# Optimization experiments

Hardware: AMD Instinct MI355X
Metric: run time of the kernel (lower is better)

## Reference

```python
import jax, jax.numpy as jnp
import numpy as np

N, E, D, L, G, C = 20000, 320000, 512, 6, 64, 10
EPS = 1e-5


def setup_inputs() -> dict:
    key = jax.random.key(0)
    ks = jax.random.split(key, 8)
    s = 0.05  # small init scale to keep activations sane across 6 layers
    x = jax.random.normal(ks[0], (N, D), jnp.float32)
    edge_index = jax.random.randint(ks[1], (2, E), 0, N, jnp.int32)
    batch = jnp.sort(jax.random.randint(ks[2], (N,), 0, G, jnp.int32))
    W_rel = jax.random.normal(ks[3], (L, D, D), jnp.float32) * s
    b_rel = jnp.zeros((L, D), jnp.float32)
    W_root = jax.random.normal(ks[4], (L, D, D), jnp.float32) * s
    gamma = jnp.ones((L, D), jnp.float32)
    beta = jnp.zeros((L, D), jnp.float32)
    lin_w = jax.random.normal(ks[5], (D, C), jnp.float32) * s
    lin_b = jnp.zeros((C,), jnp.float32)
    return {"x": x, "edge_index": edge_index, "batch": batch,
            "W_rel": W_rel, "b_rel": b_rel, "W_root": W_root,
            "gamma": gamma, "beta": beta, "lin_w": lin_w, "lin_b": lin_b}


def reference(x, edge_index, batch, W_rel, b_rel, W_root, gamma, beta, lin_w, lin_b):
    # PyG GraphConv (aggr='add'): out = segment_sum(x[src] -> dst) @ W_rel + b_rel + x @ W_root
    src, dst = edge_index[0], edge_index[1]
    n = x.shape[0]
    for l in range(W_rel.shape[0]):  # 6 structurally identical layers
        agg = jax.ops.segment_sum(x[src], dst, num_segments=n)  # [N, D]
        h = agg @ W_rel[l] + b_rel[l] + x @ W_root[l]
        # BatchNorm1d in training mode: biased batch statistics over nodes
        mu = jnp.mean(h, axis=0)
        var = jnp.mean(jnp.square(h - mu), axis=0)
        x = jax.nn.relu((h - mu) * jax.lax.rsqrt(var + EPS) * gamma[l] + beta[l])
    # global_mean_pool over per-node graph ids
    sums = jax.ops.segment_sum(x, batch, num_segments=G)              # [G, D]
    counts = jax.ops.segment_sum(jnp.ones((n,), x.dtype), batch, num_segments=G)
    pooled = sums / jnp.maximum(counts, 1.0)[:, None]
    return pooled @ lin_w + lin_b  # [G, C]
```

## Files before the change

### kernel.cpp

```cpp
#include <hip/hip_runtime.h>


typedef unsigned short u16;
typedef unsigned int u32;
typedef __attribute__((ext_vector_type(8))) short bf16x8;
typedef __attribute__((ext_vector_type(16))) float f32x16;
typedef __attribute__((ext_vector_type(2))) float f32x2;

#define DFEAT 512
#define KDIM 1024
#define NLAYER 6
#define NGRAPH 64
#define NCLS 10
#define BN_EPS 1e-5f
#define NBUCKET 1024

__device__ __forceinline__ float bf_lo(u32 u) { union { u32 i; float f; } v; v.i = u << 16; return v.f; }
__device__ __forceinline__ float bf_hi(u32 u) { union { u32 i; float f; } v; v.i = u & 0xFFFF0000u; return v.f; }
__device__ __forceinline__ u16 f2bf(float f) {
  union { float f; u32 i; } v; v.f = f;
  u32 r = v.i + 0x7FFFu + ((v.i >> 16) & 1u);
  return (u16)(r >> 16);
}
__device__ __forceinline__ u32 pack2(float lo, float hi) {
  return (u32)f2bf(lo) | ((u32)f2bf(hi) << 16);
}

__device__ __forceinline__ void gload_lds16(const u16* g, u16* lds_base) {
  __builtin_amdgcn_global_load_lds(
      (const __attribute__((address_space(1))) u32*)g,
      (__attribute__((address_space(3))) u32*)lds_base, 16, 0, 0);
}

__global__ void prep_kernel(const int* __restrict__ ei, int* __restrict__ counts, int E,
                            const float* __restrict__ Wrel, const float* __restrict__ Wroot,
                            u16* __restrict__ Wt,
                            const float* __restrict__ x, u16* __restrict__ A, int M,
                            int histB, int wB) {
  __shared__ float tile[64][65];
  int b = blockIdx.x;
  int tid = threadIdx.x;
  if (b < histB) {
    int e = b * 256 + tid;
    if (e < E) atomicAdd(&counts[ei[E + e]], 1);
  } else if (b < histB + wB) {
    int t = b - histB;
    int l = t >> 7;
    int tt = t & 127;
    int k0 = (tt >> 3) << 6;
    int n0 = (tt & 7) << 6;
    int rr = tid >> 4;
    int c4 = (tid & 15) << 2;
#pragma unroll
    for (int i = 0; i < 4; i++) {
      int k = k0 + i * 16 + rr;
      const float* src = (k < DFEAT)
          ? &Wrel[((size_t)l * DFEAT + k) * DFEAT + n0 + c4]
          : &Wroot[((size_t)l * DFEAT + (k - DFEAT)) * DFEAT + n0 + c4];
      float4 v = *(const float4*)src;
      float* d = &tile[i * 16 + rr][c4];
      d[0] = v.x; d[1] = v.y; d[2] = v.z; d[3] = v.w;
    }
    __syncthreads();
    int nr = tid >> 3;
    int kc = (tid & 7) << 3;
#pragma unroll
    for (int i = 0; i < 2; i++) {
      int nl = i * 32 + nr;
      uint4 o;
      o.x = pack2(tile[kc + 0][nl], tile[kc + 1][nl]);
      o.y = pack2(tile[kc + 2][nl], tile[kc + 3][nl]);
      o.z = pack2(tile[kc + 4][nl], tile[kc + 5][nl]);
      o.w = pack2(tile[kc + 6][nl], tile[kc + 7][nl]);
      *(uint4*)&Wt[(size_t)(l * DFEAT + n0 + nl) * KDIM + k0 + kc] = o;
    }
  } else {
    int idx = (b - histB - wB) * 256 + tid;
    int row = idx >> 7;
    int c4 = (idx & 127) * 4;
    if (row < M) {
      float4 v = *(const float4*)&x[(size_t)row * DFEAT + c4];
      uint2 o; o.x = pack2(v.x, v.y); o.y = pack2(v.z, v.w);
      *(uint2*)&A[(size_t)row * KDIM + DFEAT + c4] = o;
    }
  }
}

__global__ __launch_bounds__(1024) void dscan_kernel(const int* __restrict__ counts,
                                                     int* __restrict__ base0,
                                                     int* __restrict__ bcur,
                                                     int* __restrict__ edgebase,
                                                     int* __restrict__ row_ptr2, int n) {
  __shared__ int hist[NBUCKET];
  __shared__ int part[NBUCKET];
  int tid = threadIdx.x;
  hist[tid] = 0;
  __syncthreads();
  for (int i = tid; i < n; i += 1024) {
    int d = counts[i]; if (d > NBUCKET - 1) d = NBUCKET - 1;
    atomicAdd(&hist[d], 1);
  }
  __syncthreads();
  int c = hist[tid];
  part[tid] = c; __syncthreads();
  int x = c;
  for (int off = 1; off < NBUCKET; off <<= 1) {
    int t = (tid >= off) ? part[tid - off] : 0;
    __syncthreads();
    x += t; part[tid] = x;
    __syncthreads();
  }
  base0[tid] = x - c;
  bcur[tid] = x - c;
  int w = c * tid;
  part[tid] = w; __syncthreads();
  int y = w;
  for (int off = 1; off < NBUCKET; off <<= 1) {
    int t = (tid >= off) ? part[tid - off] : 0;
    __syncthreads();
    y += t; part[tid] = y;
    __syncthreads();
  }
  edgebase[tid] = y - w;
  if (tid == NBUCKET - 1) row_ptr2[n] = y;
}

__global__ __launch_bounds__(256) void rank_kernel(const int* __restrict__ counts,
                                                   const int* __restrict__ base0,
                                                   int* __restrict__ bcur,
                                                   const int* __restrict__ edgebase,
                                                   int* __restrict__ perm,
                                                   int* __restrict__ row_ptr2,
                                                   int* __restrict__ cursor2, int n) {
  __shared__ int hb[NBUCKET];
  __shared__ int hstart[NBUCKET];
  int tid = threadIdx.x;
  for (int d = tid; d < NBUCKET; d += 256) hb[d] = 0;
  __syncthreads();
  int row = blockIdx.x * 256 + tid;
  bool valid = (row < n);
  int deg = 0, j = 0;
  if (valid) {
    deg = counts[row]; if (deg > NBUCKET - 1) deg = NBUCKET - 1;
    j = atomicAdd(&hb[deg], 1);
  }
  __syncthreads();
  for (int d = tid; d < NBUCKET; d += 256) {
    int c = hb[d];
    hstart[d] = c ? atomicAdd(&bcur[d], c) : 0;
  }
  __syncthreads();
  if (valid) {
    int rnk = hstart[deg] + j;
    int jj = rnk - base0[deg];
    int v = edgebase[deg] + jj * deg;
    perm[rnk] = row;
    row_ptr2[rnk] = v;
    cursor2[row] = v;
  }
}

__global__ void scatter_kernel(const int* __restrict__ ei, int* __restrict__ cursor2,
                               int* __restrict__ csr2, int E) {
  int e = blockIdx.x * 256 + threadIdx.x;
  if (e < E) {
    int d = ei[E + e];
    int pos = atomicAdd(&cursor2[d], 1);
    csr2[pos] = ei[e];
  }
}

template <bool FUSED>
__device__ __forceinline__ void acc8(uint4 v, const f32x2* sc, const f32x2* sh, f32x2* a) {
  f32x2 t0 = {bf_lo(v.x), bf_hi(v.x)};
  f32x2 t1 = {bf_lo(v.y), bf_hi(v.y)};
  f32x2 t2 = {bf_lo(v.z), bf_hi(v.z)};
  f32x2 t3 = {bf_lo(v.w), bf_hi(v.w)};
  if constexpr (FUSED) {
    f32x2 z = {0.f, 0.f};
    a[0] += __builtin_elementwise_max(t0 * sc[0] + sh[0], z);
    a[1] += __builtin_elementwise_max(t1 * sc[1] + sh[1], z);
    a[2] += __builtin_elementwise_max(t2 * sc[2] + sh[2], z);
    a[3] += __builtin_elementwise_max(t3 * sc[3] + sh[3], z);
  } else {
    a[0] += t0; a[1] += t1; a[2] += t2; a[3] += t3;
  }
}

#define GCAP 1536
template <bool FUSED>
__global__ __launch_bounds__(256) void gather_kernel(u16* __restrict__ A,
                                                     const u16* __restrict__ Hb,
                                                     const float* __restrict__ sums,
                                                     const float* __restrict__ gamma,
                                                     const float* __restrict__ beta,
                                                     const int* __restrict__ row_ptr2,
                                                     const int* __restrict__ csr2,
                                                     const int* __restrict__ perm,
                                                     int n, float invN) {
  __shared__ int sidx[GCAP];
  int b = blockIdx.x;
  int slice = b & 7;
  int grp = b >> 3;
  int tid = threadIdx.x;
  int r0 = grp * 32;
  int rend = (r0 + 32 < n) ? (r0 + 32) : n;
  int wbeg = row_ptr2[r0], wend = row_ptr2[rend];
  int cnt = wend - wbeg;
  bool lds_ok = (cnt <= GCAP);
  if (lds_ok)
    for (int t = tid; t < cnt; t += 256) sidx[t] = csr2[wbeg + t];
  __syncthreads();

  int wid = tid >> 6, lane = tid & 63;
  int dsub = lane >> 3, fl = lane & 7;
  int rnk = r0 + wid * 8 + dsub;
  if (rnk >= n) return;
  int dst = perm[rnk];
  int cc = slice * 64 + fl * 8;
  f32x2 sc2[4], sh2[4];
  if constexpr (FUSED) {
#pragma unroll
    for (int j = 0; j < 8; j++) {
      int c = cc + j;
      float mu = sums[c] * invN;
      float var = sums[DFEAT + c] * invN - mu * mu;
      float s = gamma[c] * rsqrtf(var + BN_EPS);
      sc2[j >> 1][j & 1] = s;
      sh2[j >> 1][j & 1] = beta[c] - mu * s;
    }
    uint4 h = *(const uint4*)&Hb[(size_t)dst * DFEAT + cc];
    f32x2 z = {0.f, 0.f};
    f32x2 e0 = __builtin_elementwise_max((f32x2){bf_lo(h.x), bf_hi(h.x)} * sc2[0] + sh2[0], z);
    f32x2 e1 = __builtin_elementwise_max((f32x2){bf_lo(h.y), bf_hi(h.y)} * sc2[1] + sh2[1], z);
    f32x2 e2 = __builtin_elementwise_max((f32x2){bf_lo(h.z), bf_hi(h.z)} * sc2[2] + sh2[2], z);
    f32x2 e3 = __builtin_elementwise_max((f32x2){bf_lo(h.w), bf_hi(h.w)} * sc2[3] + sh2[3], z);
    uint4 o;
    o.x = pack2(e0[0], e0[1]); o.y = pack2(e1[0], e1[1]);
    o.z = pack2(e2[0], e2[1]); o.w = pack2(e3[0], e3[1]);
    *(uint4*)&A[(size_t)dst * KDIM + DFEAT + cc] = o;
  }
  const u16* Sx = FUSED ? (Hb + cc) : (A + DFEAT + cc);
  const size_t RS = FUSED ? DFEAT : KDIM;
  int db = row_ptr2[rnk], de = row_ptr2[rnk + 1];
  f32x2 a[4] = {};
  if (lds_ok) {
    int e = db - wbeg, ee = de - wbeg;
    for (; e + 7 < ee; e += 8) {
      int s0 = sidx[e + 0], s1 = sidx[e + 1], s2 = sidx[e + 2], s3 = sidx[e + 3];
      int s4 = sidx[e + 4], s5 = sidx[e + 5], s6 = sidx[e + 6], s7 = sidx[e + 7];
      uint4 v0 = *(const uint4*)&Sx[(size_t)s0 * RS];
      uint4 v1 = *(const uint4*)&Sx[(size_t)s1 * RS];
      uint4 v2 = *(const uint4*)&Sx[(size_t)s2 * RS];
      uint4 v3 = *(const uint4*)&Sx[(size_t)s3 * RS];
      uint4 v4 = *(const uint4*)&Sx[(size_t)s4 * RS];
      uint4 v5 = *(const uint4*)&Sx[(size_t)s5 * RS];
      uint4 v6 = *(const uint4*)&Sx[(size_t)s6 * RS];
      uint4 v7 = *(const uint4*)&Sx[(size_t)s7 * RS];
      acc8<FUSED>(v0, sc2, sh2, a); acc8<FUSED>(v1, sc2, sh2, a);
      acc8<FUSED>(v2, sc2, sh2, a); acc8<FUSED>(v3, sc2, sh2, a);
      acc8<FUSED>(v4, sc2, sh2, a); acc8<FUSED>(v5, sc2, sh2, a);
      acc8<FUSED>(v6, sc2, sh2, a); acc8<FUSED>(v7, sc2, sh2, a);
    }
    for (; e < ee; ++e) {
      uint4 v = *(const uint4*)&Sx[(size_t)sidx[e] * RS];
      acc8<FUSED>(v, sc2, sh2, a);
    }
  } else {
    for (int e = db; e < de; ++e) {
      uint4 v = *(const uint4*)&Sx[(size_t)csr2[e] * RS];
      acc8<FUSED>(v, sc2, sh2, a);
    }
  }
  uint4 o;
  o.x = pack2(a[0][0], a[0][1]); o.y = pack2(a[1][0], a[1][1]);
  o.z = pack2(a[2][0], a[2][1]); o.w = pack2(a[3][0], a[3][1]);
  *(uint4*)&A[(size_t)dst * KDIM + cc] = o;
}

#define BM 128
#define BN 128
#define BK 64
#define CSTR 132
__global__ __launch_bounds__(256, 4) void gemm_kernel(const u16* __restrict__ A,
                                                      const u16* __restrict__ Bt,
                                                      const float* __restrict__ bias,
                                                      u16* __restrict__ Hb,
                                                      float* __restrict__ sums, int M) {
  const int lin = blockIdx.x;
  const int bx = ((lin >> 5) << 3) + (lin & 7);
  const int by = (lin >> 3) & 3;
  const int m0 = bx * BM;
  if (m0 >= M) return;
  const int n0 = by * BN;

  __shared__ u16 smem[BM * CSTR];
  __shared__ float sred[2 * BN];
  u16* As = smem;
  u16* Bs = smem + BM * BK;
  const int tid = threadIdx.x;
  const int wid = tid >> 6, lane = tid & 63;
  const int wm = wid >> 1, wn = wid & 1;
  const int l31 = lane & 31, half = lane >> 5;

  if (tid < 2 * BN) sred[tid] = 0.f;

  const int dr = lane >> 3;
  const int gcol = ((lane & 7) ^ dr) * 8;
  int arow[4], brow[4];
#pragma unroll
  for (int t = 0; t < 4; t++) {
    int r = wid * 32 + t * 8 + dr;
    int ar = m0 + r; if (ar >= M) ar = M - 1;
    arow[t] = ar;
    brow[t] = n0 + r;
  }

  f32x16 acc[2][2] = {};

  for (int k0 = 0; k0 < KDIM; k0 += BK) {
    __syncthreads();
#pragma unroll
    for (int t = 0; t < 4; t++)
      gload_lds16(&A[(size_t)arow[t] * KDIM + k0 + gcol], &As[(wid * 32 + t * 8) * BK]);
#pragma unroll
    for (int t = 0; t < 4; t++)
      gload_lds16(&Bt[(size_t)brow[t] * KDIM + k0 + gcol], &Bs[(wid * 32 + t * 8) * BK]);
    __syncthreads();
#pragma unroll
    for (int ks = 0; ks < 4; ks++) {
      int slot = ((ks * 2 + half) ^ (l31 & 7)) * 8;
      bf16x8 a0 = *(const bf16x8*)&As[(wm * 64 + l31) * BK + slot];
      bf16x8 a1 = *(const bf16x8*)&As[(wm * 64 + 32 + l31) * BK + slot];
      bf16x8 b0 = *(const bf16x8*)&Bs[(wn * 64 + l31) * BK + slot];
      bf16x8 b1 = *(const bf16x8*)&Bs[(wn * 64 + 32 + l31) * BK + slot];
      acc[0][0] = __builtin_amdgcn_mfma_f32_32x32x16_bf16(a0, b0, acc[0][0], 0, 0, 0);
      acc[0][1] = __builtin_amdgcn_mfma_f32_32x32x16_bf16(a0, b1, acc[0][1], 0, 0, 0);
      acc[1][0] = __builtin_amdgcn_mfma_f32_32x32x16_bf16(a1, b0, acc[1][0], 0, 0, 0);
      acc[1][1] = __builtin_amdgcn_mfma_f32_32x32x16_bf16(a1, b1, acc[1][1], 0, 0, 0);
    }
  }

  __syncthreads();

#pragma unroll
  for (int nt = 0; nt < 2; nt++) {
    int colt = wn * 64 + nt * 32 + l31;
    float bv = bias[n0 + colt];
    float s = 0.f, s2 = 0.f;
#pragma unroll
    for (int mt = 0; mt < 2; mt++) {
      int rbase = wm * 64 + mt * 32 + half * 4;
#pragma unroll
      for (int reg = 0; reg < 16; reg++) {
        int rowt = rbase + (reg & 3) + 8 * (reg >> 2);
        float v = acc[mt][nt][reg] + bv;
        smem[rowt * CSTR + colt] = f2bf(v);
        if (m0 + rowt < M) { s += v; s2 += v * v; }
      }
    }
    s  += __shfl_xor(s, 32);
    s2 += __shfl_xor(s2, 32);
    if (half == 0) {
      atomicAdd(&sred[colt], s);
      atomicAdd(&sred[BN + colt], s2);
    }
  }
  __syncthreads();

  const int rsub = tid >> 4;
  const int c8 = (tid & 15) * 8;
#pragma unroll
  for (int it = 0; it < 8; it++) {
    int rowt = it * 16 + rsub;
    int grow = m0 + rowt;
    if (grow < M) {
      uint4 v = *(const uint4*)&smem[rowt * CSTR + c8];
      *(uint4*)&Hb[(size_t)grow * DFEAT + n0 + c8] = v;
    }
  }
  if (tid < BN) {
    atomicAdd(&sums[n0 + tid], sred[tid]);
    atomicAdd(&sums[DFEAT + n0 + tid], sred[BN + tid]);
  }
}

__device__ __forceinline__ int lower_bound_dev(const int* a, int n, int v) {
  int lo = 0, hi = n;
  while (lo < hi) { int mid = (lo + hi) >> 1; if (a[mid] < v) lo = mid + 1; else hi = mid; }
  return lo;
}

__global__ __launch_bounds__(1024) void pool_kernel(const u16* __restrict__ Hb,
                                                    const float* __restrict__ sums,
                                                    const float* __restrict__ gamma,
                                                    const float* __restrict__ beta,
                                                    const int* __restrict__ batch,
                                                    float* __restrict__ pooled, int n, float invN) {
  __shared__ float red[DFEAT];
  int g = blockIdx.x;
  int tid = threadIdx.x;
  if (tid < DFEAT) red[tid] = 0.f;
  int lo = lower_bound_dev(batch, n, g);
  int hi = lower_bound_dev(batch, n, g + 1);
  int rowOff = tid >> 6, lane = tid & 63;
  int c0 = lane * 8;
  float sc[8], sh[8];
#pragma unroll
  for (int j = 0; j < 8; j++) {
    int c = c0 + j;
    float mu = sums[c] * invN;
    float var = sums[DFEAT + c] * invN - mu * mu;
    float s = gamma[c] * rsqrtf(var + BN_EPS);
    sc[j] = s;
    sh[j] = beta[c] - mu * s;
  }
  float a[8] = {};
  for (int r = lo + rowOff; r < hi; r += 16) {
    uint4 v = *(const uint4*)&Hb[(size_t)r * DFEAT + c0];
    float e0 = bf_lo(v.x), e1 = bf_hi(v.x), e2 = bf_lo(v.y), e3 = bf_hi(v.y);
    float e4 = bf_lo(v.z), e5 = bf_hi(v.z), e6 = bf_lo(v.w), e7 = bf_hi(v.w);
    a[0] += fmaxf(e0 * sc[0] + sh[0], 0.f); a[1] += fmaxf(e1 * sc[1] + sh[1], 0.f);
    a[2] += fmaxf(e2 * sc[2] + sh[2], 0.f); a[3] += fmaxf(e3 * sc[3] + sh[3], 0.f);
    a[4] += fmaxf(e4 * sc[4] + sh[4], 0.f); a[5] += fmaxf(e5 * sc[5] + sh[5], 0.f);
    a[6] += fmaxf(e6 * sc[6] + sh[6], 0.f); a[7] += fmaxf(e7 * sc[7] + sh[7], 0.f);
  }
  __syncthreads();
#pragma unroll
  for (int j = 0; j < 8; j++) atomicAdd(&red[c0 + j], a[j]);
  __syncthreads();
  if (tid < DFEAT) pooled[g * DFEAT + tid] = red[tid] / fmaxf((float)(hi - lo), 1.0f);
}

__global__ __launch_bounds__(64) void final_kernel(const float* __restrict__ pooled,
                                                   const float* __restrict__ lin_w,
                                                   const float* __restrict__ lin_b,
                                                   float* __restrict__ out) {
  int g = blockIdx.x;
  int lane = threadIdx.x;
  float acc[NCLS] = {};
  float4 p0 = *(const float4*)&pooled[g * DFEAT + lane * 8];
  float4 p1 = *(const float4*)&pooled[g * DFEAT + lane * 8 + 4];
  float pv[8] = {p0.x, p0.y, p0.z, p0.w, p1.x, p1.y, p1.z, p1.w};
#pragma unroll
  for (int j = 0; j < 8; j++) {
    int k = lane * 8 + j;
#pragma unroll
    for (int c = 0; c < NCLS; c++) acc[c] += pv[j] * lin_w[k * NCLS + c];
  }
#pragma unroll
  for (int off = 32; off > 0; off >>= 1)
#pragma unroll
    for (int c = 0; c < NCLS; c++) acc[c] += __shfl_down(acc[c], off);
  if (lane == 0)
#pragma unroll
    for (int c = 0; c < NCLS; c++) out[g * NCLS + c] = acc[c] + lin_b[c];
}

extern "C" void kernel_launch(void* const* d_in, const int* in_sizes, int n_in,
                              void* d_out, int out_size, void* d_ws, size_t ws_size,
                              hipStream_t stream) {
  const float* x      = (const float*)d_in[0];
  const int*   ei     = (const int*)d_in[1];
  const int*   batch  = (const int*)d_in[2];
  const float* W_rel  = (const float*)d_in[3];
  const float* b_rel  = (const float*)d_in[4];
  const float* W_root = (const float*)d_in[5];
  const float* gamma  = (const float*)d_in[6];
  const float* beta   = (const float*)d_in[7];
  const float* lin_w  = (const float*)d_in[8];
  const float* lin_b  = (const float*)d_in[9];
  float* out = (float*)d_out;

  const int N = in_sizes[0] / DFEAT;
  const int E = in_sizes[1] / 2;

  char* p = (char*)d_ws;
  u16*   A        = (u16*)p;    p += (size_t)N * KDIM * 2;
  u16*   Hb       = (u16*)p;    p += (size_t)N * DFEAT * 2;
  u16*   Wt       = (u16*)p;    p += (size_t)NLAYER * DFEAT * KDIM * 2;
  int*   row_ptr2 = (int*)p;    p += ((size_t)(N + 1) * 4 + 15) / 16 * 16;
  int*   counts   = (int*)p;    p += (size_t)N * 4;
  int*   cursor2  = (int*)p;    p += (size_t)N * 4;
  int*   perm     = (int*)p;    p += (size_t)N * 4;
  int*   csr2     = (int*)p;    p += (size_t)E * 4;
  int*   base0    = (int*)p;    p += (size_t)NBUCKET * 4;
  int*   bcur     = (int*)p;    p += (size_t)NBUCKET * 4;
  int*   edgebase = (int*)p;    p += (size_t)NBUCKET * 4;
  float* sums     = (float*)p;  p += (size_t)NLAYER * 2 * DFEAT * 4;
  float* pooled   = (float*)p;  p += (size_t)NGRAPH * DFEAT * 4;

  const float invN = 1.0f / (float)N;

  hipMemsetAsync(counts, 0, (size_t)N * 4, stream);
  hipMemsetAsync(sums, 0, (size_t)NLAYER * 2 * DFEAT * 4, stream);

  const int histB = (E + 255) / 256;
  const int wB = NLAYER * 128;
  const int xB = (N * 128 + 255) / 256;
  prep_kernel<<<histB + wB + xB, 256, 0, stream>>>(ei, counts, E, W_rel, W_root, Wt,
                                                   x, A, N, histB, wB);
  dscan_kernel<<<1, 1024, 0, stream>>>(counts, base0, bcur, edgebase, row_ptr2, N);
  rank_kernel<<<(N + 255) / 256, 256, 0, stream>>>(counts, base0, bcur, edgebase,
                                                   perm, row_ptr2, cursor2, N);
  scatter_kernel<<<(E + 255) / 256, 256, 0, stream>>>(ei, cursor2, csr2, E);

  const int ngrp8 = ((N + 31) / 32) * 8;
  const int gtiles = (((N + BM - 1) / BM + 7) / 8) * 8 * 4;

  for (int l = 0; l < NLAYER; ++l) {
    float* sums_l = sums + (size_t)l * 2 * DFEAT;
    if (l == 0)
      gather_kernel<false><<<ngrp8, 256, 0, stream>>>(A, Hb, nullptr, nullptr, nullptr,
                                                      row_ptr2, csr2, perm, N, invN);
    else
      gather_kernel<true><<<ngrp8, 256, 0, stream>>>(A, Hb,
          sums + (size_t)(l - 1) * 2 * DFEAT,
          gamma + (size_t)(l - 1) * DFEAT, beta + (size_t)(l - 1) * DFEAT,
          row_ptr2, csr2, perm, N, invN);
    gemm_kernel<<<gtiles, 256, 0, stream>>>(A, Wt + (size_t)l * DFEAT * KDIM,
                                            b_rel + (size_t)l * DFEAT, Hb, sums_l, N);
  }

  pool_kernel<<<NGRAPH, 1024, 0, stream>>>(Hb, sums + (size_t)(NLAYER - 1) * 2 * DFEAT,
                                           gamma + (size_t)(NLAYER - 1) * DFEAT,
                                           beta + (size_t)(NLAYER - 1) * DFEAT,
                                           batch, pooled, N, invN);
  final_kernel<<<NGRAPH, 64, 0, stream>>>(pooled, lin_w, lin_b, out);
}
```

Baseline: 562.3 us.

## Double-buffer GEMM LDS tiles and reverse gather block order

Measured after the change: 621.7 us. 1.11x slower.

```diff
diff --git a/kernel.cpp b/kernel.cpp
--- a/kernel.cpp
+++ b/kernel.cpp
@@ -201,7 +201,8 @@
   __shared__ int sidx[GCAP];
   int b = blockIdx.x;
   int slice = b & 7;
-  int grp = b >> 3;
+  int nGrp = (n + 31) >> 5;
+  int grp = nGrp - 1 - (b >> 3);
   int tid = threadIdx.x;
   int r0 = grp * 32;
   int rend = (r0 + 32 < n) ? (r0 + 32) : n;
@@ -282,7 +283,8 @@
 #define BN 128
 #define BK 64
 #define CSTR 132
-__global__ __launch_bounds__(256, 4) void gemm_kernel(const u16* __restrict__ A,
+#define BUFSZ (BM * BK + BN * BK)
+__global__ __launch_bounds__(256, 2) void gemm_kernel(const u16* __restrict__ A,
                                                       const u16* __restrict__ Bt,
                                                       const float* __restrict__ bias,
                                                       u16* __restrict__ Hb,
@@ -294,10 +296,8 @@
   if (m0 >= M) return;
   const int n0 = by * BN;
 
-  __shared__ u16 smem[BM * CSTR];
+  __shared__ u16 smem[2 * BUFSZ];
   __shared__ float sred[2 * BN];
-  u16* As = smem;
-  u16* Bs = smem + BM * BK;
   const int tid = threadIdx.x;
   const int wid = tid >> 6, lane = tid & 63;
   const int wm = wid >> 1, wn = wid & 1;
@@ -318,30 +318,42 @@
 
   f32x16 acc[2][2] = {};
 
-  for (int k0 = 0; k0 < KDIM; k0 += BK) {
-    __syncthreads();
-#pragma unroll
-    for (int t = 0; t < 4; t++)
-      gload_lds16(&A[(size_t)arow[t] * KDIM + k0 + gcol], &As[(wid * 32 + t * 8) * BK]);
-#pragma unroll
-    for (int t = 0; t < 4; t++)
-      gload_lds16(&Bt[(size_t)brow[t] * KDIM + k0 + gcol], &Bs[(wid * 32 + t * 8) * BK]);
-    __syncthreads();
+#pragma unroll
+  for (int t = 0; t < 4; t++) {
+    gload_lds16(&A[(size_t)arow[t] * KDIM + gcol], &smem[(wid * 32 + t * 8) * BK]);
+    gload_lds16(&Bt[(size_t)brow[t] * KDIM + gcol], &smem[BM * BK + (wid * 32 + t * 8) * BK]);
+  }
+  __syncthreads();
+
+  const int NIT = KDIM / BK;
+  for (int it = 0; it < NIT; ++it) {
+    const int cur = it & 1;
+    if (it + 1 < NIT) {
+      const int k1 = (it + 1) * BK;
+      u16* Asn = &smem[(cur ^ 1) * BUFSZ];
+      u16* Bsn = Asn + BM * BK;
+#pragma unroll
+      for (int t = 0; t < 4; t++) {
+        gload_lds16(&A[(size_t)arow[t] * KDIM + k1 + gcol], &Asn[(wid * 32 + t * 8) * BK]);
+        gload_lds16(&Bt[(size_t)brow[t] * KDIM + k1 + gcol], &Bsn[(wid * 32 + t * 8) * BK]);
+      }
+    }
+    const u16* Asc = &smem[cur * BUFSZ];
+    const u16* Bsc = Asc + BM * BK;
 #pragma unroll
     for (int ks = 0; ks < 4; ks++) {
       int slot = ((ks * 2 + half) ^ (l31 & 7)) * 8;
-      bf16x8 a0 = *(const bf16x8*)&As[(wm * 64 + l31) * BK + slot];
-      bf16x8 a1 = *(const bf16x8*)&As[(wm * 64 + 32 + l31) * BK + slot];
-      bf16x8 b0 = *(const bf16x8*)&Bs[(wn * 64 + l31) * BK + slot];
-      bf16x8 b1 = *(const bf16x8*)&Bs[(wn * 64 + 32 + l31) * BK + slot];
+      bf16x8 a0 = *(const bf16x8*)&Asc[(wm * 64 + l31) * BK + slot];
+      bf16x8 a1 = *(const bf16x8*)&Asc[(wm * 64 + 32 + l31) * BK + slot];
+      bf16x8 b0 = *(const bf16x8*)&Bsc[(wn * 64 + l31) * BK + slot];
+      bf16x8 b1 = *(const bf16x8*)&Bsc[(wn * 64 + 32 + l31) * BK + slot];
       acc[0][0] = __builtin_amdgcn_mfma_f32_32x32x16_bf16(a0, b0, acc[0][0], 0, 0, 0);
       acc[0][1] = __builtin_amdgcn_mfma_f32_32x32x16_bf16(a0, b1, acc[0][1], 0, 0, 0);
       acc[1][0] = __builtin_amdgcn_mfma_f32_32x32x16_bf16(a1, b0, acc[1][0], 0, 0, 0);
       acc[1][1] = __builtin_amdgcn_mfma_f32_32x32x16_bf16(a1, b1, acc[1][1], 0, 0, 0);
     }
-  }
-
-  __syncthreads();
+    __syncthreads();
+  }
 
 #pragma unroll
   for (int nt = 0; nt < 2; nt++) {
```

## Widen GEMM tile to 128x256 with 512 threads and reverse gather block order

Applied to the files above, without the earlier changes.

New measurement: 586.2 us. +4.2%, slower.

```diff
diff --git a/kernel.cpp b/kernel.cpp
--- a/kernel.cpp
+++ b/kernel.cpp
@@ -201,7 +201,8 @@
   __shared__ int sidx[GCAP];
   int b = blockIdx.x;
   int slice = b & 7;
-  int grp = b >> 3;
+  int nGrp = (n + 31) >> 5;
+  int grp = nGrp - 1 - (b >> 3);
   int tid = threadIdx.x;
   int r0 = grp * 32;
   int rend = (r0 + 32 < n) ? (r0 + 32) : n;
@@ -279,50 +280,51 @@
 }
 
 #define BM 128
-#define BN 128
+#define BN 256
 #define BK 64
 #define CSTR 132
-__global__ __launch_bounds__(256, 4) void gemm_kernel(const u16* __restrict__ A,
+__global__ __launch_bounds__(512, 4) void gemm_kernel(const u16* __restrict__ A,
                                                       const u16* __restrict__ Bt,
                                                       const float* __restrict__ bias,
                                                       u16* __restrict__ Hb,
                                                       float* __restrict__ sums, int M) {
   const int lin = blockIdx.x;
-  const int bx = ((lin >> 5) << 3) + (lin & 7);
-  const int by = (lin >> 3) & 3;
+  const int bx = ((lin >> 4) << 3) + (lin & 7);
+  const int by = (lin >> 3) & 1;
   const int m0 = bx * BM;
   if (m0 >= M) return;
   const int n0 = by * BN;
 
-  __shared__ u16 smem[BM * CSTR];
+  __shared__ u16 smem[BM * BK + BN * BK];
   __shared__ float sred[2 * BN];
   u16* As = smem;
   u16* Bs = smem + BM * BK;
   const int tid = threadIdx.x;
   const int wid = tid >> 6, lane = tid & 63;
-  const int wm = wid >> 1, wn = wid & 1;
+  const int wm = wid >> 2, wn = wid & 3;
   const int l31 = lane & 31, half = lane >> 5;
 
   if (tid < 2 * BN) sred[tid] = 0.f;
 
   const int dr = lane >> 3;
   const int gcol = ((lane & 7) ^ dr) * 8;
-  int arow[4], brow[4];
-#pragma unroll
-  for (int t = 0; t < 4; t++) {
-    int r = wid * 32 + t * 8 + dr;
+  int arow[2], brow[4];
+#pragma unroll
+  for (int t = 0; t < 2; t++) {
+    int r = wid * 16 + t * 8 + dr;
     int ar = m0 + r; if (ar >= M) ar = M - 1;
     arow[t] = ar;
-    brow[t] = n0 + r;
-  }
+  }
+#pragma unroll
+  for (int t = 0; t < 4; t++) brow[t] = n0 + wid * 32 + t * 8 + dr;
 
   f32x16 acc[2][2] = {};
 
   for (int k0 = 0; k0 < KDIM; k0 += BK) {
     __syncthreads();
 #pragma unroll
-    for (int t = 0; t < 4; t++)
-      gload_lds16(&A[(size_t)arow[t] * KDIM + k0 + gcol], &As[(wid * 32 + t * 8) * BK]);
+    for (int t = 0; t < 2; t++)
+      gload_lds16(&A[(size_t)arow[t] * KDIM + k0 + gcol], &As[(wid * 16 + t * 8) * BK]);
 #pragma unroll
     for (int t = 0; t < 4; t++)
       gload_lds16(&Bt[(size_t)brow[t] * KDIM + k0 + gcol], &Bs[(wid * 32 + t * 8) * BK]);
@@ -344,45 +346,49 @@
   __syncthreads();
 
 #pragma unroll
-  for (int nt = 0; nt < 2; nt++) {
-    int colt = wn * 64 + nt * 32 + l31;
-    float bv = bias[n0 + colt];
-    float s = 0.f, s2 = 0.f;
-#pragma unroll
-    for (int mt = 0; mt < 2; mt++) {
-      int rbase = wm * 64 + mt * 32 + half * 4;
-#pragma unroll
-      for (int reg = 0; reg < 16; reg++) {
-        int rowt = rbase + (reg & 3) + 8 * (reg >> 2);
-        float v = acc[mt][nt][reg] + bv;
-        smem[rowt * CSTR + colt] = f2bf(v);
-        if (m0 + rowt < M) { s += v; s2 += v * v; }
+  for (int hpass = 0; hpass < 2; hpass++) {
+    if ((wn >> 1) == hpass) {
+#pragma unroll
+      for (int nt = 0; nt < 2; nt++) {
+        int coltC = wn * 64 + nt * 32 + l31;
+        int coltL = coltC - hpass * 128;
+        float bv = bias[n0 + coltC];
+        float s = 0.f, s2 = 0.f;
+#pragma unroll
+        for (int mt = 0; mt < 2; mt++) {
+          int rbase = wm * 64 + mt * 32 + half * 4;
+#pragma unroll
+          for (int reg = 0; reg < 16; reg++) {
+            int rowt = rbase + (reg & 3) + 8 * (reg >> 2);
+            float v = acc[mt][nt][reg] + bv;
+            smem[rowt * CSTR + coltL] = f2bf(v);
+            if (m0 + rowt < M) { s += v; s2 += v * v; }
+          }
+        }
+        s  += __shfl_xor(s, 32);
+        s2 += __shfl_xor(s2, 32);
+        if (half == 0) {
+          atomicAdd(&sred[coltC], s);
+          atomicAdd(&sred[BN + coltC], s2);
+        }
       }
     }
-    s  += __shfl_xor(s, 32);
-    s2 += __shfl_xor(s2, 32);
-    if (half == 0) {
-      atomicAdd(&sred[colt], s);
-      atomicAdd(&sred[BN + colt], s2);
-    }
-  }
-  __syncthreads();
-
-  const int rsub = tid >> 4;
-  const int c8 = (tid & 15) * 8;
-#pragma unroll
-  for (int it = 0; it < 8; it++) {
-    int rowt = it * 16 + rsub;
-    int grow = m0 + rowt;
-    if (grow < M) {
-      uint4 v = *(const uint4*)&smem[rowt * CSTR + c8];
-      *(uint4*)&Hb[(size_t)grow * DFEAT + n0 + c8] = v;
-    }
-  }
-  if (tid < BN) {
-    atomicAdd(&sums[n0 + tid], sred[tid]);
-    atomicAdd(&sums[DFEAT + n0 + tid], sred[BN + tid]);
-  }
+    __syncthreads();
+    const int rsub = tid >> 4;
+    const int c8 = (tid & 15) * 8;
+#pragma unroll
+    for (int it = 0; it < 4; it++) {
+      int rowt = it * 32 + rsub;
+      int grow = m0 + rowt;
+      if (grow < M) {
+        uint4 v = *(const uint4*)&smem[rowt * CSTR + c8];
+        *(uint4*)&Hb[(size_t)grow * DFEAT + n0 + hpass * 128 + c8] = v;
+      }
+    }
+    __syncthreads();
+  }
+  if (tid < BN) atomicAdd(&sums[n0 + tid], sred[tid]);
+  else if (tid < 2 * BN) atomicAdd(&sums[DFEAT + n0 + tid - BN], sred[tid]);
 }
 
 __device__ __forceinline__ int lower_bound_dev(const int* a, int n, int v) {
@@ -506,7 +512,7 @@
   scatter_kernel<<<(E + 255) / 256, 256, 0, stream>>>(ei, cursor2, csr2, E);
 
   const int ngrp8 = ((N + 31) / 32) * 8;
-  const int gtiles = (((N + BM - 1) / BM + 7) / 8) * 8 * 4;
+  const int gtiles = (((N + BM - 1) / BM + 7) / 8) * 8 * 2;
 
   for (int l = 0; l < NLAYER; ++l) {
     float* sums_l = sums + (size_t)l * 2 * DFEAT;
@@ -518,7 +524,7 @@
           sums + (size_t)(l - 1) * 2 * DFEAT,
           gamma + (size_t)(l - 1) * DFEAT, beta + (size_t)(l - 1) * DFEAT,
           row_ptr2, csr2, perm, N, invN);
-    gemm_kernel<<<gtiles, 256, 0, stream>>>(A, Wt + (size_t)l * DFEAT * KDIM,
+    gemm_kernel<<<gtiles, 512, 0, stream>>>(A, Wt + (size_t)l * DFEAT * KDIM,
                                             b_rel + (size_t)l * DFEAT, Hb, sums_l, N);
   }
 
```

## Add row-per-wave gather variant for alternate layers, reverse block order, fuse final linear into pool

Applied to the files above, without the earlier changes.

New measurement: 588.3 us. +4.6%, slower.

```diff
diff --git a/kernel.cpp b/kernel.cpp
--- a/kernel.cpp
+++ b/kernel.cpp
@@ -201,7 +201,8 @@
   __shared__ int sidx[GCAP];
   int b = blockIdx.x;
   int slice = b & 7;
-  int grp = b >> 3;
+  int nGrp = (n + 31) >> 5;
+  int grp = nGrp - 1 - (b >> 3);
   int tid = threadIdx.x;
   int r0 = grp * 32;
   int rend = (r0 + 32 < n) ? (r0 + 32) : n;
@@ -278,6 +279,92 @@
   *(uint4*)&A[(size_t)dst * KDIM + cc] = o;
 }
 
+#define RCAP 512
+__global__ __launch_bounds__(256) void gather_row_kernel(u16* __restrict__ A,
+                                                         const u16* __restrict__ Hb,
+                                                         const float* __restrict__ sums,
+                                                         const float* __restrict__ gamma,
+                                                         const float* __restrict__ beta,
+                                                         const int* __restrict__ row_ptr2,
+                                                         const int* __restrict__ csr2,
+                                                         const int* __restrict__ perm,
+                                                         int n, float invN) {
+  __shared__ int sidx[RCAP];
+  int b = blockIdx.x;
+  int tid = threadIdx.x;
+  int rhi = n - 4 * b;
+  int rlo = rhi - 4; if (rlo < 0) rlo = 0;
+  int wbeg = row_ptr2[rlo], wend = row_ptr2[rhi];
+  int cnt = wend - wbeg;
+  bool lds_ok = (cnt <= RCAP);
+  if (lds_ok)
+    for (int t = tid; t < cnt; t += 256) sidx[t] = csr2[wbeg + t];
+  __syncthreads();
+
+  int wid = tid >> 6, lane = tid & 63;
+  int rnk = rlo + wid;
+  if (rnk >= rhi) return;
+  int dst = perm[rnk];
+  int cc = lane * 8;
+  f32x2 sc2[4], sh2[4];
+#pragma unroll
+  for (int j = 0; j < 8; j++) {
+    int c = cc + j;
+    float mu = sums[c] * invN;
+    float var = sums[DFEAT + c] * invN - mu * mu;
+    float s = gamma[c] * rsqrtf(var + BN_EPS);
+    sc2[j >> 1][j & 1] = s;
+    sh2[j >> 1][j & 1] = beta[c] - mu * s;
+  }
+  {
+    uint4 h = *(const uint4*)&Hb[(size_t)dst * DFEAT + cc];
+    f32x2 z = {0.f, 0.f};
+    f32x2 e0 = __builtin_elementwise_max((f32x2){bf_lo(h.x), bf_hi(h.x)} * sc2[0] + sh2[0], z);
+    f32x2 e1 = __builtin_elementwise_max((f32x2){bf_lo(h.y), bf_hi(h.y)} * sc2[1] + sh2[1], z);
+    f32x2 e2 = __builtin_elementwise_max((f32x2){bf_lo(h.z), bf_hi(h.z)} * sc2[2] + sh2[2], z);
+    f32x2 e3 = __builtin_elementwise_max((f32x2){bf_lo(h.w), bf_hi(h.w)} * sc2[3] + sh2[3], z);
+    uint4 o;
+    o.x = pack2(e0[0], e0[1]); o.y = pack2(e1[0], e1[1]);
+    o.z = pack2(e2[0], e2[1]); o.w = pack2(e3[0], e3[1]);
+    *(uint4*)&A[(size_t)dst * KDIM + DFEAT + cc] = o;
+  }
+  const u16* Sx = Hb + cc;
+  int db = row_ptr2[rnk], de = row_ptr2[rnk + 1];
+  f32x2 a[4] = {};
+  if (lds_ok) {
+    int e = db - wbeg, ee = de - wbeg;
+    for (; e + 7 < ee; e += 8) {
+      int s0 = sidx[e + 0], s1 = sidx[e + 1], s2 = sidx[e + 2], s3 = sidx[e + 3];
+      int s4 = sidx[e + 4], s5 = sidx[e + 5], s6 = sidx[e + 6], s7 = sidx[e + 7];
+      uint4 v0 = *(const uint4*)&Sx[(size_t)s0 * DFEAT];
+      uint4 v1 = *(const uint4*)&Sx[(size_t)s1 * DFEAT];
+      uint4 v2 = *(const uint4*)&Sx[(size_t)s2 * DFEAT];
+      uint4 v3 = *(const uint4*)&Sx[(size_t)s3 * DFEAT];
+      uint4 v4 = *(const uint4*)&Sx[(size_t)s4 * DFEAT];
+      uint4 v5 = *(const uint4*)&Sx[(size_t)s5 * DFEAT];
+      uint4 v6 = *(const uint4*)&Sx[(size_t)s6 * DFEAT];
+      uint4 v7 = *(const uint4*)&Sx[(size_t)s7 * DFEAT];
+      acc8<true>(v0, sc2, sh2, a); acc8<true>(v1, sc2, sh2, a);
+      acc8<true>(v2, sc2, sh2, a); acc8<true>(v3, sc2, sh2, a);
+      acc8<true>(v4, sc2, sh2, a); acc8<true>(v5, sc2, sh2, a);
+      acc8<true>(v6, sc2, sh2, a); acc8<true>(v7, sc2, sh2, a);
+    }
+    for (; e < ee; ++e) {
+      uint4 v = *(const uint4*)&Sx[(size_t)sidx[e] * DFEAT];
+      acc8<true>(v, sc2, sh2, a);
+    }
+  } else {
+    for (int e = db; e < de; ++e) {
+      uint4 v = *(const uint4*)&Sx[(size_t)csr2[e] * DFEAT];
+      acc8<true>(v, sc2, sh2, a);
+    }
+  }
+  uint4 o;
+  o.x = pack2(a[0][0], a[0][1]); o.y = pack2(a[1][0], a[1][1]);
+  o.z = pack2(a[2][0], a[2][1]); o.w = pack2(a[3][0], a[3][1]);
+  *(uint4*)&A[(size_t)dst * KDIM + cc] = o;
+}
+
 #define BM 128
 #define BN 128
 #define BK 64
@@ -396,11 +483,15 @@
                                                     const float* __restrict__ gamma,
                                                     const float* __restrict__ beta,
                                                     const int* __restrict__ batch,
-                                                    float* __restrict__ pooled, int n, float invN) {
+                                                    const float* __restrict__ lin_w,
+                                                    const float* __restrict__ lin_b,
+                                                    float* __restrict__ out, int n, float invN) {
   __shared__ float red[DFEAT];
+  __shared__ float outc[NCLS];
   int g = blockIdx.x;
   int tid = threadIdx.x;
   if (tid < DFEAT) red[tid] = 0.f;
+  if (tid >= DFEAT && tid < DFEAT + NCLS) outc[tid - DFEAT] = 0.f;
   int lo = lower_bound_dev(batch, n, g);
   int hi = lower_bound_dev(batch, n, g + 1);
   int rowOff = tid >> 6, lane = tid & 63;
@@ -429,32 +520,22 @@
 #pragma unroll
   for (int j = 0; j < 8; j++) atomicAdd(&red[c0 + j], a[j]);
   __syncthreads();
-  if (tid < DFEAT) pooled[g * DFEAT + tid] = red[tid] / fmaxf((float)(hi - lo), 1.0f);
-}
-
-__global__ __launch_bounds__(64) void final_kernel(const float* __restrict__ pooled,
-                                                   const float* __restrict__ lin_w,
-                                                   const float* __restrict__ lin_b,
-                                                   float* __restrict__ out) {
-  int g = blockIdx.x;
-  int lane = threadIdx.x;
-  float acc[NCLS] = {};
-  float4 p0 = *(const float4*)&pooled[g * DFEAT + lane * 8];
-  float4 p1 = *(const float4*)&pooled[g * DFEAT + lane * 8 + 4];
-  float pv[8] = {p0.x, p0.y, p0.z, p0.w, p1.x, p1.y, p1.z, p1.w};
-#pragma unroll
-  for (int j = 0; j < 8; j++) {
-    int k = lane * 8 + j;
-#pragma unroll
-    for (int c = 0; c < NCLS; c++) acc[c] += pv[j] * lin_w[k * NCLS + c];
-  }
-#pragma unroll
-  for (int off = 32; off > 0; off >>= 1)
-#pragma unroll
-    for (int c = 0; c < NCLS; c++) acc[c] += __shfl_down(acc[c], off);
-  if (lane == 0)
-#pragma unroll
-    for (int c = 0; c < NCLS; c++) out[g * NCLS + c] = acc[c] + lin_b[c];
+  float invCnt = 1.0f / fmaxf((float)(hi - lo), 1.0f);
+  if (tid < DFEAT) {
+    float pv = red[tid] * invCnt;
+    float pc[NCLS];
+#pragma unroll
+    for (int c = 0; c < NCLS; c++) pc[c] = pv * lin_w[tid * NCLS + c];
+#pragma unroll
+    for (int off = 32; off > 0; off >>= 1)
+#pragma unroll
+      for (int c = 0; c < NCLS; c++) pc[c] += __shfl_down(pc[c], off);
+    if ((tid & 63) == 0)
+#pragma unroll
+      for (int c = 0; c < NCLS; c++) atomicAdd(&outc[c], pc[c]);
+  }
+  __syncthreads();
+  if (tid < NCLS) out[g * NCLS + tid] = outc[tid] + lin_b[tid];
 }
 
 extern "C" void kernel_launch(void* const* d_in, const int* in_sizes, int n_in,
@@ -488,7 +569,6 @@
   int*   bcur     = (int*)p;    p += (size_t)NBUCKET * 4;
   int*   edgebase = (int*)p;    p += (size_t)NBUCKET * 4;
   float* sums     = (float*)p;  p += (size_t)NLAYER * 2 * DFEAT * 4;
-  float* pooled   = (float*)p;  p += (size_t)NGRAPH * DFEAT * 4;
 
   const float invN = 1.0f / (float)N;
 
@@ -506,18 +586,25 @@
   scatter_kernel<<<(E + 255) / 256, 256, 0, stream>>>(ei, cursor2, csr2, E);
 
   const int ngrp8 = ((N + 31) / 32) * 8;
+  const int nrow4 = (N + 3) / 4;
   const int gtiles = (((N + BM - 1) / BM + 7) / 8) * 8 * 4;
 
   for (int l = 0; l < NLAYER; ++l) {
     float* sums_l = sums + (size_t)l * 2 * DFEAT;
-    if (l == 0)
+    if (l == 0) {
       gather_kernel<false><<<ngrp8, 256, 0, stream>>>(A, Hb, nullptr, nullptr, nullptr,
                                                       row_ptr2, csr2, perm, N, invN);
-    else
+    } else if (l == 2 || l == 4) {
+      gather_row_kernel<<<nrow4, 256, 0, stream>>>(A, Hb,
+          sums + (size_t)(l - 1) * 2 * DFEAT,
+          gamma + (size_t)(l - 1) * DFEAT, beta + (size_t)(l - 1) * DFEAT,
+          row_ptr2, csr2, perm, N, invN);
+    } else {
       gather_kernel<true><<<ngrp8, 256, 0, stream>>>(A, Hb,
           sums + (size_t)(l - 1) * 2 * DFEAT,
           gamma + (size_t)(l - 1) * DFEAT, beta + (size_t)(l - 1) * DFEAT,
           row_ptr2, csr2, perm, N, invN);
+    }
     gemm_kernel<<<gtiles, 256, 0, stream>>>(A, Wt + (size_t)l * DFEAT * KDIM,
                                             b_rel + (size_t)l * DFEAT, Hb, sums_l, N);
   }
@@ -525,6 +612,5 @@
   pool_kernel<<<NGRAPH, 1024, 0, stream>>>(Hb, sums + (size_t)(NLAYER - 1) * 2 * DFEAT,
                                            gamma + (size_t)(NLAYER - 1) * DFEAT,
                                            beta + (size_t)(NLAYER - 1) * DFEAT,
-                                           batch, pooled, N, invN);
-  final_kernel<<<NGRAPH, 64, 0, stream>>>(pooled, lin_w, lin_b, out);
-}
+                                           batch, lin_w, lin_b, out, N, invN);
+}
```
